# Performance work log

Hardware: AMD Instinct MI355X
Metric: run time of the kernel (lower is better)

The kernel has to match this reference:

```python
import jax, jax.numpy as jnp
import numpy as np

H = 16          # num_heads
RMS_EPS = 1.1920928955078125e-07  # torch.finfo(float32).eps (F.rms_norm default)
NORM_EPS = 1e-12                  # F.normalize default eps


def _rms_norm(t):
    # F.rms_norm without weight: t / sqrt(mean(t^2) + eps)
    ms = jnp.mean(t * t, axis=-1, keepdims=True)
    return t * jax.lax.rsqrt(ms + RMS_EPS)


def setup_inputs() -> dict:
    key = jax.random.key(0)
    k1, k2, k3 = jax.random.split(key, 3)
    B, N, C = 2, 2048, 1024
    x = jax.random.normal(k1, (B, N, C), dtype=jnp.float32)
    # nn.Linear weights are (out_features, in_features); scale like kaiming-uniform-ish
    w_qkv = jax.random.normal(k2, (3 * C, C), dtype=jnp.float32) * (C ** -0.5)
    w_proj = jax.random.normal(k3, (C, C), dtype=jnp.float32) * (C ** -0.5)
    return {"x": x, "w_qkv": w_qkv, "w_proj": w_proj}


def reference(x, w_qkv, w_proj):
    B, N, C = x.shape
    D = C // H
    scale = D ** -0.5
    qkv = x @ w_qkv.T                                  # (B,N,3C)
    qkv = qkv.reshape(B, N, 3, H, D)
    q = qkv[:, :, 0].transpose(0, 2, 1, 3)             # (B,H,N,D)
    k = qkv[:, :, 1].transpose(0, 2, 1, 3)
    v = qkv[:, :, 2].transpose(0, 2, 1, 3)
    q = _rms_norm(q)
    k = _rms_norm(k)
    attn = jnp.einsum('bhnd,bhmd->bhnm', q, k) * scale  # (B,H,N,N)
    attn = jax.nn.softmax(attn, axis=-1)
    y = jnp.einsum('bhnm,bhmd->bhnd', attn, v)          # (B,H,N,D)
    # xsa: subtract projection of y onto normalized v
    vnorm = jnp.linalg.norm(v, axis=-1, keepdims=True)
    Vn = v / jnp.maximum(vnorm, NORM_EPS)
    y = y - jnp.sum(y * Vn, axis=-1, keepdims=True) * Vn
    out = y.transpose(0, 2, 1, 3).reshape(B, N, C)
    return out @ w_proj.T
```

## Files before the change

### kernel.cpp

```cpp
#include <hip/hip_runtime.h>
#include <hip/hip_bf16.h>
#include <cstdint>

#define RMS_EPS 1.1920928955078125e-07f
#define SMAX 12.0f

typedef __bf16 bf16;
typedef __attribute__((ext_vector_type(8))) __bf16 bf16x8;
typedef __attribute__((ext_vector_type(4))) __bf16 bf16x4;
typedef __attribute__((ext_vector_type(4))) float f32x4;
typedef __attribute__((ext_vector_type(16))) float f32x16;
typedef unsigned int u32;
typedef __attribute__((ext_vector_type(4))) u32 u32x4;

__device__ __forceinline__ void gload16(const bf16* g, bf16* l) {
  __builtin_amdgcn_global_load_lds(
      (__attribute__((address_space(1))) void*)(g),
      (__attribute__((address_space(3))) void*)(l), 16, 0, 0);
}

__device__ __forceinline__ float fexp2(float x) {
#if __has_builtin(__builtin_amdgcn_exp2f)
  return __builtin_amdgcn_exp2f(x);
#else
  return exp2f(x);
#endif
}

__device__ __forceinline__ u32 pack2(float a, float b) {
  unsigned short xa = __builtin_bit_cast(unsigned short, (bf16)a);
  unsigned short xb = __builtin_bit_cast(unsigned short, (bf16)b);
  return (u32)xa | ((u32)xb << 16);
}

__global__ __launch_bounds__(256) void cvt3_kernel(
    const float* __restrict__ x, const float* __restrict__ wq, const float* __restrict__ wp,
    bf16* __restrict__ xo, bf16* __restrict__ wqo, bf16* __restrict__ wpo) {
  int i = blockIdx.x * 256 + threadIdx.x;
  const float* s; bf16* d; int off;
  if (i < 524288) { s = x; d = xo; off = i; }
  else if (i < 917504) { s = wq; d = wqo; off = i - 524288; }
  else { s = wp; d = wpo; off = i - 917504; }
  const float4* s4 = (const float4*)s;
  float4 a = s4[off * 2], b = s4[off * 2 + 1];
  bf16x8 o;
  o[0] = (bf16)a.x; o[1] = (bf16)a.y; o[2] = (bf16)a.z; o[3] = (bf16)a.w;
  o[4] = (bf16)b.x; o[5] = (bf16)b.y; o[6] = (bf16)b.z; o[7] = (bf16)b.w;
  *(bf16x8*)(d + off * 8) = o;
}

template <int MODE, int MINW>
__global__ __launch_bounds__(256, MINW) void gemm_bt(
    const bf16* __restrict__ A, const bf16* __restrict__ B,
    float* __restrict__ Cout, int Ncols,
    bf16* __restrict__ Qb, bf16* __restrict__ Kb, bf16* __restrict__ VtG,
    float* __restrict__ vninv) {
  union ShG {
    struct { bf16 As[128 * 64]; bf16 Bs[128 * 64]; } s;
    bf16 T[128 * 136];
  };
  __shared__ ShG shg;
  bf16* As = shg.s.As;
  bf16* Bs = shg.s.Bs;

  const int tid = threadIdx.x;
  const int wave = tid >> 6, lane = tid & 63;
  const int l15 = lane & 15, g = lane >> 4;
  const int nwg = gridDim.x * gridDim.y;
  const int wg0 = blockIdx.y * gridDim.x + blockIdx.x;
  const int wg = (wg0 & 7) * (nwg >> 3) + (wg0 >> 3);
  const int m0 = (wg / gridDim.x) * 128, n0 = (wg % gridDim.x) * 128;
  const int wr = wave >> 1, wc = wave & 1;

  f32x4 acc[4][4] = {};

  for (int k0 = 0; k0 < 1024; k0 += 64) {
    __syncthreads();
#pragma unroll
    for (int i = 0; i < 4; ++i) {
      const int gid = (i * 4 + wave) * 64 + lane;
      const int row = gid >> 3, gk = gid & 7;
      const int srcoff = k0 + ((gk ^ (row & 7)) << 3);
      gload16(A + (m0 + row) * 1024 + srcoff, As + (i * 4 + wave) * 512);
      gload16(B + (n0 + row) * 1024 + srcoff, Bs + (i * 4 + wave) * 512);
    }
    __syncthreads();
#pragma unroll
    for (int kc = 0; kc < 2; ++kc) {
      bf16x8 af[4], bfb[4];
#pragma unroll
      for (int mi = 0; mi < 4; ++mi) {
        const int row = wr * 64 + mi * 16 + l15;
        af[mi] = *(const bf16x8*)&As[row * 64 + (((kc * 4 + g) ^ (l15 & 7)) << 3)];
      }
#pragma unroll
      for (int ni = 0; ni < 4; ++ni) {
        const int row = wc * 64 + ni * 16 + l15;
        bfb[ni] = *(const bf16x8*)&Bs[row * 64 + (((kc * 4 + g) ^ (l15 & 7)) << 3)];
      }
#pragma unroll
      for (int mi = 0; mi < 4; ++mi)
#pragma unroll
        for (int ni = 0; ni < 4; ++ni)
          acc[mi][ni] = __builtin_amdgcn_mfma_f32_16x16x32_bf16(af[mi], bfb[ni], acc[mi][ni], 0, 0, 0);
    }
  }

  if (MODE == 0) {
#pragma unroll
    for (int mi = 0; mi < 4; ++mi) {
      const int mrow = m0 + wr * 64 + mi * 16 + g * 4;
#pragma unroll
      for (int r = 0; r < 4; ++r) {
        float* cp = Cout + (long)(mrow + r) * Ncols + n0 + wc * 64 + l15;
#pragma unroll
        for (int ni = 0; ni < 4; ++ni) cp[ni * 16] = acc[mi][ni][r];
      }
    }
  } else {
    const int blk_which = n0 >> 10;
    const int ncol = n0 + wc * 64;
    const int h = (ncol >> 6) & 15;

    if (blk_which == 2) {
#pragma unroll
      for (int mi = 0; mi < 4; ++mi) {
#pragma unroll
        for (int r = 0; r < 4; ++r) {
          float ss = 0.f;
#pragma unroll
          for (int ni = 0; ni < 4; ++ni) ss += acc[mi][ni][r] * acc[mi][ni][r];
          ss += __shfl_xor(ss, 1); ss += __shfl_xor(ss, 2);
          ss += __shfl_xor(ss, 4); ss += __shfl_xor(ss, 8);
          if (l15 == 0) {
            const int m = m0 + wr * 64 + mi * 16 + g * 4 + r;
            const int b = m >> 11, nseq = m & 2047;
            vninv[(b * 16 + h) * 2048 + nseq] = 1.0f / fmaxf(sqrtf(ss), 1e-12f);
          }
        }
      }
      __syncthreads();
#pragma unroll
      for (int mi = 0; mi < 4; ++mi)
#pragma unroll
        for (int ni = 0; ni < 4; ++ni) {
          bf16x4 v4;
#pragma unroll
          for (int r = 0; r < 4; ++r) v4[r] = (bf16)acc[mi][ni][r];
          *(bf16x4*)&shg.T[(wc * 64 + ni * 16 + l15) * 136 + wr * 64 + mi * 16 + g * 4] = v4;
        }
      __syncthreads();
      const int c = tid >> 1, half = tid & 1;
      const int gcol = n0 + c;
      const int hh = (gcol >> 6) & 15, d = gcol & 63;
      const int mb = m0 >> 11, nseq0 = m0 & 2047;
      bf16* dst = VtG + ((long)(mb * 16 + hh) * 64 + d) * 2048 + nseq0 + half * 64;
      const bf16* src = &shg.T[c * 136 + half * 64];
#pragma unroll
      for (int i = 0; i < 8; ++i)
        *(bf16x8*)(dst + i * 8) = *(const bf16x8*)(src + i * 8);
    } else {
      float scv[4][4];
#pragma unroll
      for (int mi = 0; mi < 4; ++mi) {
#pragma unroll
        for (int r = 0; r < 4; ++r) {
          float ss = 0.f;
#pragma unroll
          for (int ni = 0; ni < 4; ++ni) ss += acc[mi][ni][r] * acc[mi][ni][r];
          ss += __shfl_xor(ss, 1); ss += __shfl_xor(ss, 2);
          ss += __shfl_xor(ss, 4); ss += __shfl_xor(ss, 8);
          const float sc = rsqrtf(ss * (1.0f / 64) + RMS_EPS);
          scv[mi][r] = (blk_which == 0) ? sc * (0.125f * 1.44269504088896340736f) : sc;
        }
      }
      __syncthreads();
#pragma unroll
      for (int mi = 0; mi < 4; ++mi)
#pragma unroll
        for (int r = 0; r < 4; ++r) {
          const float sc = scv[mi][r];
#pragma unroll
          for (int ni = 0; ni < 4; ++ni)
            shg.T[(wr * 64 + mi * 16 + g * 4 + r) * 136 + wc * 64 + ni * 16 + l15] =
                (bf16)(acc[mi][ni][r] * sc);
        }
      __syncthreads();
      bf16* QK = (blk_which == 0) ? Qb : Kb;
      const int c8 = tid & 7, chh = (tid >> 3) & 1, r0 = tid >> 4;
      const int hh = ((n0 + chh * 64) >> 6) & 15;
#pragma unroll
      for (int p = 0; p < 8; ++p) {
        const int rr = r0 + p * 16;
        const int m = m0 + rr;
        const int bq = m >> 11, nseq = m & 2047;
        *(bf16x8*)(QK + ((long)(bq * 16 + hh) * 2048 + nseq) * 64 + c8 * 8) =
            *(const bf16x8*)&shg.T[rr * 136 + chh * 64 + c8 * 8];
      }
    }
  }
}

__global__ __launch_bounds__(256, 2) void attn_kernel(
    const bf16* __restrict__ Qb, const bf16* __restrict__ Kb, const bf16* __restrict__ VtG,
    const float* __restrict__ vninv, bf16* __restrict__ Yb) {
  __shared__ bf16 Ks[2][128 * 64];
  __shared__ bf16 Vt[2][64 * 128];

  const int tid = threadIdx.x;
  const int wq = tid >> 6;
  const int lane = tid & 63;
  const int l31 = lane & 31, hi = lane >> 5;
  const int wg = (blockIdx.x & 7) * (gridDim.x >> 3) + (blockIdx.x >> 3);
  const int bh = wg >> 4, qb = wg & 15;
  const int b = bh >> 4, h = bh & 15;
  const long off = (long)bh * (2048 * 64);
  const bf16* Qp = Qb + off;
  const bf16* Kp = Kb + off;
  const bf16* VtP = VtG + (long)bh * 64 * 2048;
  const int qrow = qb * 128 + wq * 32 + l31;

  bf16x8 qf[4];
#pragma unroll
  for (int kc = 0; kc < 4; ++kc)
    qf[kc] = *(const bf16x8*)&Qp[qrow * 64 + kc * 16 + hi * 8];

  f32x16 o[2] = {};
  f32x16 lacc = {};
  f32x16 minit;
#pragma unroll
  for (int r = 0; r < 16; ++r) minit[r] = -SMAX;

  int koff[4], voff[4];
#pragma unroll
  for (int i = 0; i < 4; ++i) {
    const int chunk = i * 4 + wq;
    const int j = chunk * 8 + (lane >> 3);
    koff[i] = j * 64 + (((lane & 7) ^ ((j ^ (j >> 3)) & 7)) << 3);
    const int d = chunk * 4 + (lane >> 4);
    voff[i] = d * 2048 + (((lane & 15) ^ ((d ^ (d >> 3)) & 7)) << 3);
  }

#pragma unroll
  for (int i = 0; i < 4; ++i) {
    const int chunk = i * 4 + wq;
    gload16(Kp + koff[i], &Ks[0][chunk * 512]);
    gload16(VtP + voff[i], &Vt[0][chunk * 512]);
  }
  __syncthreads();

  int cur = 0;
  for (int it = 0; it < 16; ++it) {
    const int kv0 = it * 128;
    if (it < 15) {
#pragma unroll
      for (int i = 0; i < 4; ++i) {
        const int chunk = i * 4 + wq;
        gload16(Kp + (kv0 + 128) * 64 + koff[i], &Ks[cur ^ 1][chunk * 512]);
        gload16(VtP + (kv0 + 128) + voff[i], &Vt[cur ^ 1][chunk * 512]);
      }
    }
    const bf16* ks = &Ks[cur][0];
    const bf16* vt = &Vt[cur][0];

    f32x16 sv[4];
    __builtin_amdgcn_s_setprio(1);
#pragma unroll
    for (int jt = 0; jt < 4; ++jt) {
      const int j = jt * 32 + l31;
      const int key = (j ^ (j >> 3)) & 7;
      {
        bf16x8 kf = *(const bf16x8*)&ks[j * 64 + ((hi ^ key) << 3)];
        sv[jt] = __builtin_amdgcn_mfma_f32_32x32x16_bf16(kf, qf[0], minit, 0, 0, 0);
      }
#pragma unroll
      for (int kc = 1; kc < 4; ++kc) {
        bf16x8 kf = *(const bf16x8*)&ks[j * 64 + (((2 * kc + hi) ^ key) << 3)];
        sv[jt] = __builtin_amdgcn_mfma_f32_32x32x16_bf16(kf, qf[kc], sv[jt], 0, 0, 0);
      }
    }
    __builtin_amdgcn_s_setprio(0);

#pragma unroll
    for (int jt = 0; jt < 4; ++jt)
#pragma unroll
      for (int r = 0; r < 16; ++r) sv[jt][r] = fexp2(sv[jt][r]);

#pragma unroll
    for (int r = 0; r < 16; ++r)
      lacc[r] += (sv[0][r] + sv[1][r]) + (sv[2][r] + sv[3][r]);

    u32 w[4][8];
#pragma unroll
    for (int jt = 0; jt < 4; ++jt)
#pragma unroll
      for (int i = 0; i < 8; ++i) w[jt][i] = pack2(sv[jt][2 * i], sv[jt][2 * i + 1]);
    bf16x8 pafr[8];
#pragma unroll
    for (int kc = 0; kc < 8; ++kc) {
      const int c = kc & 1, jt = kc >> 1;
      const u32 z1 = hi ? w[jt][4 * c + 0] : w[jt][4 * c + 2];
      const u32 z2 = hi ? w[jt][4 * c + 1] : w[jt][4 * c + 3];
      const u32 r1 = __shfl_xor(z1, 32);
      const u32 r2 = __shfl_xor(z2, 32);
      u32x4 pv;
      pv[0] = hi ? r1 : w[jt][4 * c + 0];
      pv[1] = hi ? r2 : w[jt][4 * c + 1];
      pv[2] = hi ? w[jt][4 * c + 2] : r1;
      pv[3] = hi ? w[jt][4 * c + 3] : r2;
      pafr[kc] = __builtin_bit_cast(bf16x8, pv);
    }

    __builtin_amdgcn_s_setprio(1);
#pragma unroll
    for (int dt = 0; dt < 2; ++dt) {
      const int d = dt * 32 + l31;
      const int key = (d ^ (d >> 3)) & 7;
#pragma unroll
      for (int kc = 0; kc < 8; ++kc) {
        bf16x8 vf = *(const bf16x8*)&vt[d * 128 + (((2 * kc + hi) ^ key) << 3)];
        o[dt] = __builtin_amdgcn_mfma_f32_32x32x16_bf16(vf, pafr[kc], o[dt], 0, 0, 0);
      }
    }
    __builtin_amdgcn_s_setprio(0);

    __syncthreads();
    cur ^= 1;
  }

  float sm[16];
#pragma unroll
  for (int r = 0; r < 16; ++r) sm[r] = lacc[r];
#pragma unroll
  for (int s2 = 8; s2 > 0; s2 >>= 1)
#pragma unroll
    for (int r = 0; r < s2; ++r) sm[r] += sm[r + s2];
  const float lrun = sm[0] + __shfl_xor(sm[0], 32);

  const float linv = 1.f / lrun;
  const float vni = vninv[bh * 2048 + qrow];
  const float cvn = vni * vni;
  const bf16* vq = VtP + qrow;
  float yv[2][16], vvf[2][16];
  float t = 0.f;
#pragma unroll
  for (int dt = 0; dt < 2; ++dt)
#pragma unroll
    for (int rr = 0; rr < 4; ++rr) {
#pragma unroll
      for (int e = 0; e < 4; ++e) {
        const int r = rr * 4 + e;
        const int d = e + 8 * rr + 4 * hi + 32 * dt;
        const float y = o[dt][r] * linv;
        const float vx = (float)vq[d * 2048];
        yv[dt][r] = y; vvf[dt][r] = vx;
        t += y * vx;
      }
    }
  t += __shfl_xor(t, 32);
  const float coef = t * cvn;
  bf16* yp = Yb + ((long)b * 2048 + qrow) * 1024 + h * 64;
#pragma unroll
  for (int dt = 0; dt < 2; ++dt)
#pragma unroll
    for (int rr = 0; rr < 4; ++rr) {
      bf16x4 y4;
#pragma unroll
      for (int e = 0; e < 4; ++e) {
        const int r = rr * 4 + e;
        y4[e] = (bf16)(yv[dt][r] - coef * vvf[dt][r]);
      }
      *(bf16x4*)&yp[dt * 32 + rr * 8 + hi * 4] = y4;
    }
}

extern "C" void kernel_launch(void* const* d_in, const int* in_sizes, int n_in,
                              void* d_out, int out_size, void* d_ws, size_t ws_size,
                              hipStream_t stream) {
  (void)in_sizes; (void)n_in; (void)out_size; (void)ws_size;
  const float* x = (const float*)d_in[0];
  const float* w_qkv = (const float*)d_in[1];
  const float* w_proj = (const float*)d_in[2];
  float* out = (float*)d_out;
  char* ws = (char*)d_ws;

  bf16* xb     = (bf16*)(ws);
  bf16* wqkvb  = (bf16*)(ws + 8388608);
  bf16* wprojb = (bf16*)(ws + 14680064);
  bf16* Qb     = (bf16*)(ws + 16777216);
  bf16* Kb     = (bf16*)(ws + 25165824);
  bf16* VtG    = (bf16*)(ws + 33554432);
  float* vninv = (float*)(ws + 41943040);
  bf16* Yb     = (bf16*)(ws + 42467328);

  cvt3_kernel<<<4096, 256, 0, stream>>>(x, w_qkv, w_proj, xb, wqkvb, wprojb);

  gemm_bt<1, 3><<<dim3(24, 32), 256, 0, stream>>>(xb, wqkvb, nullptr, 3072,
                                                  Qb, Kb, VtG, vninv);
  attn_kernel<<<512, 256, 0, stream>>>(Qb, Kb, VtG, vninv, Yb);
  gemm_bt<0, 2><<<dim3(8, 32), 256, 0, stream>>>(Yb, wprojb, out, 1024,
                                                 nullptr, nullptr, nullptr, nullptr);
}
```

Measured before the change: 123.4 us.

## Split attention over two KV halves with a separate merge kernel

The attention kernel is split along the key/value sequence into two halves, doubling the grid to 1024 blocks. Shared-memory tiles shrink to 64 keys and launch bounds rise to 4 blocks per SM to raise occupancy. Each half writes unnormalized bf16 partial outputs plus row sums to workspace. A new merge kernel combines them, normalizes, and applies the xsa projection subtraction. In exchange it adds an extra launch, extra global traffic, and bf16 rounding of the unnormalized partials.

```diff
diff --git a/kernel.cpp b/kernel.cpp
--- a/kernel.cpp
+++ b/kernel.cpp
@@ -201,23 +201,23 @@
   }
 }
 
-__global__ __launch_bounds__(256, 2) void attn_kernel(
+__global__ __launch_bounds__(256, 4) void attn_split_kernel(
     const bf16* __restrict__ Qb, const bf16* __restrict__ Kb, const bf16* __restrict__ VtG,
-    const float* __restrict__ vninv, bf16* __restrict__ Yb) {
-  __shared__ bf16 Ks[2][128 * 64];
-  __shared__ bf16 Vt[2][64 * 128];
+    bf16* __restrict__ P0, bf16* __restrict__ P1, float* __restrict__ Lp) {
+  __shared__ bf16 Ks[2][64 * 64];
+  __shared__ bf16 Vt[2][64 * 64];
 
   const int tid = threadIdx.x;
   const int wq = tid >> 6;
   const int lane = tid & 63;
   const int l31 = lane & 31, hi = lane >> 5;
   const int wg = (blockIdx.x & 7) * (gridDim.x >> 3) + (blockIdx.x >> 3);
-  const int bh = wg >> 4, qb = wg & 15;
+  const int bh = wg >> 5, qb = (wg >> 1) & 15, half = wg & 1;
   const int b = bh >> 4, h = bh & 15;
   const long off = (long)bh * (2048 * 64);
   const bf16* Qp = Qb + off;
-  const bf16* Kp = Kb + off;
-  const bf16* VtP = VtG + (long)bh * 64 * 2048;
+  const bf16* Kp = Kb + off + (long)(half * 1024) * 64;
+  const bf16* VtP = VtG + (long)bh * 64 * 2048 + half * 1024;
   const int qrow = qb * 128 + wq * 32 + l31;
 
   bf16x8 qf[4];
@@ -227,22 +227,20 @@
 
   f32x16 o[2] = {};
   f32x16 lacc = {};
-  f32x16 minit;
-#pragma unroll
-  for (int r = 0; r < 16; ++r) minit[r] = -SMAX;
-
-  int koff[4], voff[4];
-#pragma unroll
-  for (int i = 0; i < 4; ++i) {
+
+  int koff[2], voff[2];
+#pragma unroll
+  for (int i = 0; i < 2; ++i) {
     const int chunk = i * 4 + wq;
-    const int j = chunk * 8 + (lane >> 3);
-    koff[i] = j * 64 + (((lane & 7) ^ ((j ^ (j >> 3)) & 7)) << 3);
-    const int d = chunk * 4 + (lane >> 4);
-    voff[i] = d * 2048 + (((lane & 15) ^ ((d ^ (d >> 3)) & 7)) << 3);
-  }
-
-#pragma unroll
-  for (int i = 0; i < 4; ++i) {
+    const int gid = chunk * 64 + lane;
+    const int row = gid >> 3, gk = gid & 7;
+    const int key = (row ^ (row >> 3)) & 7;
+    koff[i] = row * 64 + ((gk ^ key) << 3);
+    voff[i] = row * 2048 + ((gk ^ key) << 3);
+  }
+
+#pragma unroll
+  for (int i = 0; i < 2; ++i) {
     const int chunk = i * 4 + wq;
     gload16(Kp + koff[i], &Ks[0][chunk * 512]);
     gload16(VtP + voff[i], &Vt[0][chunk * 512]);
@@ -251,30 +249,30 @@
 
   int cur = 0;
   for (int it = 0; it < 16; ++it) {
-    const int kv0 = it * 128;
+    const int kv0 = it * 64;
     if (it < 15) {
 #pragma unroll
-      for (int i = 0; i < 4; ++i) {
+      for (int i = 0; i < 2; ++i) {
         const int chunk = i * 4 + wq;
-        gload16(Kp + (kv0 + 128) * 64 + koff[i], &Ks[cur ^ 1][chunk * 512]);
-        gload16(VtP + (kv0 + 128) + voff[i], &Vt[cur ^ 1][chunk * 512]);
+        gload16(Kp + (kv0 + 64) * 64 + koff[i], &Ks[cur ^ 1][chunk * 512]);
+        gload16(VtP + (kv0 + 64) + voff[i], &Vt[cur ^ 1][chunk * 512]);
       }
     }
     const bf16* ks = &Ks[cur][0];
     const bf16* vt = &Vt[cur][0];
 
-    f32x16 sv[4];
+    f32x16 sv[2];
+#pragma unroll
+    for (int jt = 0; jt < 2; ++jt)
+#pragma unroll
+      for (int r = 0; r < 16; ++r) sv[jt][r] = -SMAX;
     __builtin_amdgcn_s_setprio(1);
 #pragma unroll
-    for (int jt = 0; jt < 4; ++jt) {
+    for (int jt = 0; jt < 2; ++jt) {
       const int j = jt * 32 + l31;
       const int key = (j ^ (j >> 3)) & 7;
-      {
-        bf16x8 kf = *(const bf16x8*)&ks[j * 64 + ((hi ^ key) << 3)];
-        sv[jt] = __builtin_amdgcn_mfma_f32_32x32x16_bf16(kf, qf[0], minit, 0, 0, 0);
-      }
-#pragma unroll
-      for (int kc = 1; kc < 4; ++kc) {
+#pragma unroll
+      for (int kc = 0; kc < 4; ++kc) {
         bf16x8 kf = *(const bf16x8*)&ks[j * 64 + (((2 * kc + hi) ^ key) << 3)];
         sv[jt] = __builtin_amdgcn_mfma_f32_32x32x16_bf16(kf, qf[kc], sv[jt], 0, 0, 0);
       }
@@ -282,22 +280,21 @@
     __builtin_amdgcn_s_setprio(0);
 
 #pragma unroll
-    for (int jt = 0; jt < 4; ++jt)
+    for (int jt = 0; jt < 2; ++jt)
 #pragma unroll
       for (int r = 0; r < 16; ++r) sv[jt][r] = fexp2(sv[jt][r]);
 
 #pragma unroll
-    for (int r = 0; r < 16; ++r)
-      lacc[r] += (sv[0][r] + sv[1][r]) + (sv[2][r] + sv[3][r]);
-
-    u32 w[4][8];
-#pragma unroll
-    for (int jt = 0; jt < 4; ++jt)
+    for (int r = 0; r < 16; ++r) lacc[r] += sv[0][r] + sv[1][r];
+
+    u32 w[2][8];
+#pragma unroll
+    for (int jt = 0; jt < 2; ++jt)
 #pragma unroll
       for (int i = 0; i < 8; ++i) w[jt][i] = pack2(sv[jt][2 * i], sv[jt][2 * i + 1]);
-    bf16x8 pafr[8];
-#pragma unroll
-    for (int kc = 0; kc < 8; ++kc) {
+    bf16x8 pafr[4];
+#pragma unroll
+    for (int kc = 0; kc < 4; ++kc) {
       const int c = kc & 1, jt = kc >> 1;
       const u32 z1 = hi ? w[jt][4 * c + 0] : w[jt][4 * c + 2];
       const u32 z2 = hi ? w[jt][4 * c + 1] : w[jt][4 * c + 3];
@@ -317,8 +314,8 @@
       const int d = dt * 32 + l31;
       const int key = (d ^ (d >> 3)) & 7;
 #pragma unroll
-      for (int kc = 0; kc < 8; ++kc) {
-        bf16x8 vf = *(const bf16x8*)&vt[d * 128 + (((2 * kc + hi) ^ key) << 3)];
+      for (int kc = 0; kc < 4; ++kc) {
+        bf16x8 vf = *(const bf16x8*)&vt[d * 64 + (((2 * kc + hi) ^ key) << 3)];
         o[dt] = __builtin_amdgcn_mfma_f32_32x32x16_bf16(vf, pafr[kc], o[dt], 0, 0, 0);
       }
     }
@@ -335,43 +332,52 @@
   for (int s2 = 8; s2 > 0; s2 >>= 1)
 #pragma unroll
     for (int r = 0; r < s2; ++r) sm[r] += sm[r + s2];
-  const float lrun = sm[0] + __shfl_xor(sm[0], 32);
-
-  const float linv = 1.f / lrun;
-  const float vni = vninv[bh * 2048 + qrow];
-  const float cvn = vni * vni;
-  const bf16* vq = VtP + qrow;
-  float yv[2][16], vvf[2][16];
-  float t = 0.f;
+  const float lpart = sm[0] + __shfl_xor(sm[0], 32);
+
+  bf16* P = half ? P1 : P0;
+  const long base = ((long)(b * 2048 + qrow)) * 1024 + h * 64;
 #pragma unroll
   for (int dt = 0; dt < 2; ++dt)
 #pragma unroll
-    for (int rr = 0; rr < 4; ++rr) {
+    for (int rr = 0; rr < 4; ++rr)
 #pragma unroll
       for (int e = 0; e < 4; ++e) {
         const int r = rr * 4 + e;
         const int d = e + 8 * rr + 4 * hi + 32 * dt;
-        const float y = o[dt][r] * linv;
-        const float vx = (float)vq[d * 2048];
-        yv[dt][r] = y; vvf[dt][r] = vx;
-        t += y * vx;
-      }
-    }
-  t += __shfl_xor(t, 32);
-  const float coef = t * cvn;
-  bf16* yp = Yb + ((long)b * 2048 + qrow) * 1024 + h * 64;
-#pragma unroll
-  for (int dt = 0; dt < 2; ++dt)
-#pragma unroll
-    for (int rr = 0; rr < 4; ++rr) {
-      bf16x4 y4;
-#pragma unroll
-      for (int e = 0; e < 4; ++e) {
-        const int r = rr * 4 + e;
-        y4[e] = (bf16)(yv[dt][r] - coef * vvf[dt][r]);
-      }
-      *(bf16x4*)&yp[dt * 32 + rr * 8 + hi * 4] = y4;
-    }
+        P[base + d] = (bf16)o[dt][r];
+      }
+  if (hi == 0) Lp[half * 65536 + bh * 2048 + qrow] = lpart;
+}
+
+__global__ __launch_bounds__(256) void attn_merge_kernel(
+    const bf16* VtG, const float* vninv, const bf16* P1, const float* Lp, bf16* Yb) {
+  const int gid = blockIdx.x * 256 + threadIdx.x;
+  const int qg = gid >> 3;
+  const int dseg = gid & 7;
+  const int bh = qg >> 11, qrow = qg & 2047;
+  const int b = bh >> 4, h = bh & 15;
+  const long base = ((long)(b * 2048 + qrow)) * 1024 + h * 64 + dseg * 8;
+
+  const bf16x8 o0 = *(const bf16x8*)(Yb + base);
+  const bf16x8 o1 = *(const bf16x8*)(P1 + base);
+  const float linv = 1.f / (Lp[qg] + Lp[65536 + qg]);
+  const bf16* vp = VtG + (long)bh * 64 * 2048 + qrow;
+
+  float y[8], v[8];
+  float t = 0.f;
+#pragma unroll
+  for (int e = 0; e < 8; ++e) {
+    y[e] = ((float)o0[e] + (float)o1[e]) * linv;
+    v[e] = (float)vp[(long)(dseg * 8 + e) * 2048];
+    t += y[e] * v[e];
+  }
+  t += __shfl_xor(t, 1); t += __shfl_xor(t, 2); t += __shfl_xor(t, 4);
+  const float vni = vninv[qg];
+  const float coef = t * vni * vni;
+  bf16x8 out;
+#pragma unroll
+  for (int e = 0; e < 8; ++e) out[e] = (bf16)(y[e] - coef * v[e]);
+  *(bf16x8*)(Yb + base) = out;
 }
 
 extern "C" void kernel_launch(void* const* d_in, const int* in_sizes, int n_in,
@@ -393,11 +399,15 @@
   float* vninv = (float*)(ws + 41943040);
   bf16* Yb     = (bf16*)(ws + 42467328);
 
+  bf16* P1  = xb;
+  float* Lp = (float*)(ws + 8388608);
+
   cvt3_kernel<<<4096, 256, 0, stream>>>(x, w_qkv, w_proj, xb, wqkvb, wprojb);
 
   gemm_bt<1, 3><<<dim3(24, 32), 256, 0, stream>>>(xb, wqkvb, nullptr, 3072,
                                                   Qb, Kb, VtG, vninv);
-  attn_kernel<<<512, 256, 0, stream>>>(Qb, Kb, VtG, vninv, Yb);
+  attn_split_kernel<<<1024, 256, 0, stream>>>(Qb, Kb, VtG, Yb, P1, Lp);
+  attn_merge_kernel<<<2048, 256, 0, stream>>>(VtG, vninv, P1, Lp, Yb);
   gemm_bt<0, 2><<<dim3(8, 32), 256, 0, stream>>>(Yb, wprojb, out, 1024,
                                                  nullptr, nullptr, nullptr, nullptr);
 }
```

Measured after the change: 161.9 us. 1.31x slower.
